# Kernel optimization log

Hardware: AMD Instinct MI355X
Metric: run time of the kernel (lower is better)

Reference implementation:

```python
import jax, jax.numpy as jnp
import numpy as np

B, S, E, H = 2, 2048, 1024, 16
DH = E // H
SCALE = 1.0 / float(np.sqrt(E))  # note: original scales by 1/sqrt(hidden_dim), not head_dim


def _icl_mask(s):
    # triu(diagonal=0) is masked (-inf): only strictly-past positions visible,
    # except (0,0) which is explicitly unmasked so row 0 attends to itself.
    m = jnp.triu(jnp.ones((s, s), dtype=bool), k=0)
    return m.at[0, 0].set(False)


def setup_inputs() -> dict:
    key = jax.random.key(0)
    ks = jax.random.split(key, 7)
    mk = lambda k, shp: jax.random.normal(k, shp, dtype=jnp.float32)
    return {
        "q": mk(ks[0], (B, S, E)),
        "k": mk(ks[1], (B, S, E)),
        "v": mk(ks[2], (B, S, E)),
        "Wq": mk(ks[3], (E, E)) * 0.02,
        "Wk": mk(ks[4], (E, E)) * 0.02,
        "Wv": mk(ks[5], (E, E)) * 0.02,
        "Wo": mk(ks[6], (E, E)) * 0.02,
    }


def reference(q, k, v, Wq, Wk, Wv, Wo):
    b, s, e = q.shape
    h, dh = H, e // H
    # projections (nn.Linear: x @ W.T), split heads -> [b, h, s, dh]
    qh = (q @ Wq.T).reshape(b, s, h, dh).transpose(0, 2, 1, 3)
    kh = (k @ Wk.T).reshape(b, s, h, dh).transpose(0, 2, 1, 3)
    vh = (v @ Wv.T).reshape(b, s, h, dh).transpose(0, 2, 1, 3)
    scores = jnp.einsum("bhsd,bhtd->bhst", qh, kh) * SCALE  # [b,h,s,s]
    scores = jnp.where(_icl_mask(s), -jnp.inf, scores)
    probs = jax.nn.softmax(scores, axis=-1)
    out = jnp.einsum("bhst,bhtd->bhsd", probs, vh)
    out = out.transpose(0, 2, 1, 3).reshape(b, s, e)
    return out @ Wo.T
```

## Files before the change

### kernel.cpp

```cpp
#include <hip/hip_runtime.h>
#include <hip/hip_bf16.h>

typedef unsigned short u16;
typedef unsigned int u32;
typedef __bf16 bf16x8 __attribute__((ext_vector_type(8)));
typedef float float4_ __attribute__((ext_vector_type(4)));

#define B_ 2
#define S_ 2048
#define E_ 1024
#define H_ 16
#define DH_ 64
#define M_ (B_*S_)
#define SCALE_ 0.03125f
#define LOG2E_ 1.4426950408889634f

__device__ __forceinline__ u16 f2bf(float f) {
    unsigned int x = __float_as_uint(f);
    x += 0x7fffu + ((x >> 16) & 1u);
    return (u16)(x >> 16);
}

template <typename T> struct raw8;
template <> struct raw8<float> { float4_ lo, hi; };
template <> struct raw8<u16>   { bf16x8 v; };

__device__ __forceinline__ raw8<float> ldr8(const float* p) {
    raw8<float> r; const float4_* q = (const float4_*)p; r.lo = q[0]; r.hi = q[1]; return r;
}
__device__ __forceinline__ raw8<u16> ldr8(const u16* p) {
    raw8<u16> r; r.v = *(const bf16x8*)p; return r;
}
__device__ __forceinline__ bf16x8 cvt8(const raw8<u16>& r) { return r.v; }
__device__ __forceinline__ bf16x8 cvt8(const raw8<float>& r) {
    union { bf16x8 v; __hip_bfloat162 h[4]; } u;
    u.h[0] = __float22bfloat162_rn(float2{r.lo[0], r.lo[1]});
    u.h[1] = __float22bfloat162_rn(float2{r.lo[2], r.lo[3]});
    u.h[2] = __float22bfloat162_rn(float2{r.hi[0], r.hi[1]});
    u.h[3] = __float22bfloat162_rn(float2{r.hi[2], r.hi[3]});
    return u.v;
}
__device__ __forceinline__ bf16x8 ld8(const u16* p) { return *(const bf16x8*)p; }

__device__ __forceinline__ void async16(u16* lds, const u16* g) {
    __builtin_amdgcn_global_load_lds(
        (const __attribute__((address_space(1))) u32*)g,
        (__attribute__((address_space(3))) u32*)lds, 16, 0, 0);
}

__global__ __launch_bounds__(256)
void convw_kernel(const float* __restrict__ Wq, const float* __restrict__ Wk,
                  const float* __restrict__ Wv, const float* __restrict__ Wo,
                  u16* __restrict__ Wqb, u16* __restrict__ Wkb,
                  u16* __restrict__ Wvb, u16* __restrict__ Wob) {
    const int which = blockIdx.y;
    const float* src = which == 0 ? Wq : which == 1 ? Wk : which == 2 ? Wv : Wo;
    u16* dst        = which == 0 ? Wqb : which == 1 ? Wkb : which == 2 ? Wvb : Wob;
    size_t off = ((size_t)blockIdx.x * 256 + threadIdx.x) * 8;
    *(bf16x8*)&dst[off] = cvt8(ldr8(&src[off]));
}

__global__ __launch_bounds__(256)
void proj_kernel(const float* __restrict__ q, const float* __restrict__ k, const float* __restrict__ v,
                 const u16* __restrict__ Wqb, const u16* __restrict__ Wkb, const u16* __restrict__ Wvb,
                 u16* __restrict__ Qh, u16* __restrict__ Kh, u16* __restrict__ Vt) {
    const int z = blockIdx.z;
    const float* A = (z == 0) ? q : (z == 1) ? k : v;
    const u16* Wb  = (z == 0) ? Wqb : (z == 1) ? Wkb : Wvb;
    u16* C         = (z == 0) ? Qh : (z == 1) ? Kh : Vt;
    const float cscale = (z == 0) ? SCALE_ : 1.0f;
    const int transV = (z == 2);
    const int bm = blockIdx.x * 128, bn = blockIdx.y * 128;

    __shared__ u16 As[128 * 32];
    __shared__ u16 Bs[128 * 32];

    const int tid  = threadIdx.x;
    const int lane = tid & 63;
    const int w    = tid >> 6;
    const int wr   = (w >> 1) * 64, wc = (w & 1) * 64;
    const int m16  = lane & 15, quad = lane >> 4, q4 = quad * 4;
    const int row0 = tid >> 2, kc0 = (tid & 3) * 8, row1 = row0 + 64;
    const int c1   = tid + 256;

    u16* bs_d0 = (u16*)((char*)Bs + (size_t)tid * 16);
    u16* bs_d1 = (u16*)((char*)Bs + (size_t)c1 * 16);
    const u16* wg0 = &Wb[(size_t)(bn + (tid >> 2)) * 1024 + (tid & 3) * 8];
    const u16* wg1 = &Wb[(size_t)(bn + (c1 >> 2)) * 1024 + (c1 & 3) * 8];

    float4_ acc[4][4];
#pragma unroll
    for (int i = 0; i < 4; i++)
#pragma unroll
        for (int j = 0; j < 4; j++) acc[i][j] = (float4_){0.f, 0.f, 0.f, 0.f};

    raw8<float> pa0 = ldr8(&A[(size_t)(bm + row0) * 1024 + kc0]);
    raw8<float> pa1 = ldr8(&A[(size_t)(bm + row1) * 1024 + kc0]);

    for (int k0 = 0; k0 < 1024; k0 += 32) {
        __syncthreads();
        async16(bs_d0, wg0 + k0);
        async16(bs_d1, wg1 + k0);
        *(bf16x8*)&As[row0 * 32 + kc0] = cvt8(pa0);
        *(bf16x8*)&As[row1 * 32 + kc0] = cvt8(pa1);
        __syncthreads();
        if (k0 + 32 < 1024) {
            pa0 = ldr8(&A[(size_t)(bm + row0) * 1024 + k0 + 32 + kc0]);
            pa1 = ldr8(&A[(size_t)(bm + row1) * 1024 + k0 + 32 + kc0]);
        }
        bf16x8 af[4], bfr[4];
#pragma unroll
        for (int rt = 0; rt < 4; rt++)
            af[rt] = *(const bf16x8*)&As[(wr + rt * 16 + m16) * 32 + quad * 8];
#pragma unroll
        for (int ct = 0; ct < 4; ct++)
            bfr[ct] = *(const bf16x8*)&Bs[(wc + ct * 16 + m16) * 32 + quad * 8];
#pragma unroll
        for (int rt = 0; rt < 4; rt++)
#pragma unroll
            for (int ct = 0; ct < 4; ct++)
                acc[rt][ct] = __builtin_amdgcn_mfma_f32_16x16x32_bf16(af[rt], bfr[ct], acc[rt][ct], 0, 0, 0);
    }

#pragma unroll
    for (int rt = 0; rt < 4; rt++)
#pragma unroll
        for (int ct = 0; ct < 4; ct++)
#pragma unroll
            for (int r = 0; r < 4; r++) {
                int row = bm + wr + rt * 16 + q4 + r;
                int col = bn + wc + ct * 16 + m16;
                u16 val = f2bf(acc[rt][ct][r] * cscale);
                if (!transV) {
                    C[(size_t)row * 1024 + col] = val;
                } else {
                    int bb = row >> 11, s = row & 2047;
                    C[((size_t)(bb * 1024 + col)) * 2048 + s] = val;
                }
            }
}

__global__ __launch_bounds__(256)
void out_kernel(const u16* __restrict__ AO, const u16* __restrict__ Wob, float* __restrict__ C) {
    const int bm = blockIdx.x * 128, bn = blockIdx.y * 64;

    __shared__ u16 As[128 * 32];
    __shared__ u16 Bs[64 * 32];

    const int tid  = threadIdx.x;
    const int lane = tid & 63;
    const int w    = tid >> 6;
    const int m16  = lane & 15, quad = lane >> 4, q4 = quad * 4;
    const int c1   = tid + 256;

    u16* as_d0 = (u16*)((char*)As + (size_t)tid * 16);
    u16* as_d1 = (u16*)((char*)As + (size_t)c1 * 16);
    u16* bs_d  = (u16*)((char*)Bs + (size_t)tid * 16);
    const u16* ag0 = &AO[(size_t)(bm + (tid >> 2)) * 1024 + (tid & 3) * 8];
    const u16* ag1 = &AO[(size_t)(bm + (c1 >> 2)) * 1024 + (c1 & 3) * 8];
    const u16* bg  = &Wob[(size_t)(bn + (tid >> 2)) * 1024 + (tid & 3) * 8];

    float4_ acc[2][4];
#pragma unroll
    for (int i = 0; i < 2; i++)
#pragma unroll
        for (int j = 0; j < 4; j++) acc[i][j] = (float4_){0.f, 0.f, 0.f, 0.f};

    for (int k0 = 0; k0 < 1024; k0 += 32) {
        __syncthreads();
        async16(as_d0, ag0 + k0);
        async16(as_d1, ag1 + k0);
        async16(bs_d,  bg  + k0);
        __syncthreads();

        bf16x8 af[2], bfr[4];
#pragma unroll
        for (int rt = 0; rt < 2; rt++)
            af[rt] = *(const bf16x8*)&As[(w * 32 + rt * 16 + m16) * 32 + quad * 8];
#pragma unroll
        for (int ct = 0; ct < 4; ct++)
            bfr[ct] = *(const bf16x8*)&Bs[(ct * 16 + m16) * 32 + quad * 8];
#pragma unroll
        for (int rt = 0; rt < 2; rt++)
#pragma unroll
            for (int ct = 0; ct < 4; ct++)
                acc[rt][ct] = __builtin_amdgcn_mfma_f32_16x16x32_bf16(af[rt], bfr[ct], acc[rt][ct], 0, 0, 0);
    }

#pragma unroll
    for (int rt = 0; rt < 2; rt++)
#pragma unroll
        for (int ct = 0; ct < 4; ct++)
#pragma unroll
            for (int r = 0; r < 4; r++) {
                int row = bm + w * 32 + rt * 16 + q4 + r;
                int col = bn + ct * 16 + m16;
                C[(size_t)row * 1024 + col] = acc[rt][ct][r];
            }
}

__device__ __forceinline__ int sw64(int row, int col) {
    return row * 64 + ((((col >> 3) ^ (row & 7)) << 3) | (col & 7));
}

__global__ __launch_bounds__(256)
void attn_kernel(const u16* __restrict__ Qh, const u16* __restrict__ Kh,
                 const u16* __restrict__ Vt, u16* __restrict__ O) {
    const int h    = blockIdx.x;
    const int pair = blockIdx.y;
    const int tqA  = pair;
    const int tqB  = 31 - pair;
    const int b    = blockIdx.z;
    const int tid  = threadIdx.x;
    const int lane = tid & 63;
    const int w    = tid >> 6;
    const int m16  = lane & 15;
    const int quad = lane >> 4;
    const int q4   = quad * 4;

    __shared__ u16 Ks[2][64 * 64];
    __shared__ u16 Vs[2][64 * 64];
    __shared__ u16 PsA[64 * 64];
    __shared__ u16 PsB[64 * 64];

    const int srow0 = tid >> 3;
    const int skc0  = (tid & 7) * 8;
    const int sblk0 = ((skc0 >> 3) ^ (srow0 & 7)) << 3;
    const int srow1 = srow0 + 32;
    const int sblk1 = ((skc0 >> 3) ^ (srow1 & 7)) << 3;

    const size_t kbase = ((size_t)(b * S_)) * E_ + h * DH_;
    const size_t vbase = ((size_t)(b * 1024 + h * DH_)) * 2048;

    bf16x8 qfA[2], qfB[2];
    {
        const u16* qa = Qh + ((size_t)(b * S_ + tqA * 64 + w * 16 + m16)) * E_ + h * DH_;
        const u16* qb = Qh + ((size_t)(b * S_ + tqB * 64 + w * 16 + m16)) * E_ + h * DH_;
        qfA[0] = ld8(qa + quad * 8);  qfA[1] = ld8(qa + 32 + quad * 8);
        qfB[0] = ld8(qb + quad * 8);  qfB[1] = ld8(qb + 32 + quad * 8);
    }

    float lA[4] = {0.f, 0.f, 0.f, 0.f}, lB[4] = {0.f, 0.f, 0.f, 0.f};
    float4_ oA[4], oB[4];
#pragma unroll
    for (int dt = 0; dt < 4; dt++) { oA[dt] = (float4_){0.f,0.f,0.f,0.f}; oB[dt] = (float4_){0.f,0.f,0.f,0.f}; }

    *(bf16x8*)&Ks[0][srow0 * 64 + sblk0] = ld8(&Kh[kbase + (size_t)srow0 * E_ + skc0]);
    *(bf16x8*)&Ks[0][srow1 * 64 + sblk1] = ld8(&Kh[kbase + (size_t)srow1 * E_ + skc0]);
    *(bf16x8*)&Vs[0][srow0 * 64 + sblk0] = ld8(&Vt[vbase + (size_t)srow0 * 2048 + skc0]);
    *(bf16x8*)&Vs[0][srow1 * 64 + sblk1] = ld8(&Vt[vbase + (size_t)srow1 * 2048 + skc0]);
    __syncthreads();

    for (int t = 0; t <= tqB; t++) {
        const int cur = t & 1;

        bf16x8 kr0, kr1, vr0, vr1;
        const bool havepf = (t < tqB);
        if (havepf) {
            const size_t ko = kbase + (size_t)((t + 1) * 64) * E_;
            kr0 = ld8(&Kh[ko + (size_t)srow0 * E_ + skc0]);
            kr1 = ld8(&Kh[ko + (size_t)srow1 * E_ + skc0]);
            vr0 = ld8(&Vt[vbase + (size_t)srow0 * 2048 + (t + 1) * 64 + skc0]);
            vr1 = ld8(&Vt[vbase + (size_t)srow1 * 2048 + (t + 1) * 64 + skc0]);
        }

        auto process = [&](const bf16x8* qf, float* l_part, float4_* o_acc,
                           u16* Ps, int tqX) {
            const u16* Kc = &Ks[cur][0];
            const u16* Vc = &Vs[cur][0];
            float4_ sc[4];
#pragma unroll
            for (int ct = 0; ct < 4; ct++) sc[ct] = (float4_){0.f,0.f,0.f,0.f};
#pragma unroll
            for (int ks = 0; ks < 2; ks++)
#pragma unroll
                for (int ct = 0; ct < 4; ct++) {
                    bf16x8 kf = *(const bf16x8*)&Kc[sw64(ct * 16 + m16, ks * 32 + quad * 8)];
                    sc[ct] = __builtin_amdgcn_mfma_f32_16x16x32_bf16(qf[ks], kf, sc[ct], 0, 0, 0);
                }

            float p[4][4];
            if (t != tqX) {
#pragma unroll
                for (int ct = 0; ct < 4; ct++)
#pragma unroll
                    for (int r = 0; r < 4; r++) {
                        float pp = exp2f(sc[ct][r] * LOG2E_);
                        p[ct][r] = pp;
                        l_part[r] += pp;
                    }
            } else {
#pragma unroll
                for (int ct = 0; ct < 4; ct++)
#pragma unroll
                    for (int r = 0; r < 4; r++) {
                        int i_loc = w * 16 + q4 + r;
                        int j_loc = ct * 16 + m16;
                        bool allow = (j_loc < i_loc) || (tqX == 0 && i_loc == 0 && j_loc == 0);
                        float pp = allow ? exp2f(sc[ct][r] * LOG2E_) : 0.f;
                        p[ct][r] = pp;
                        l_part[r] += pp;
                    }
            }

#pragma unroll
            for (int ct = 0; ct < 4; ct++)
#pragma unroll
                for (int r = 0; r < 4; r++)
                    Ps[sw64(w * 16 + q4 + r, ct * 16 + m16)] = f2bf(p[ct][r]);

#pragma unroll
            for (int ks = 0; ks < 2; ks++) {
                bf16x8 pf = *(const bf16x8*)&Ps[sw64(w * 16 + m16, ks * 32 + quad * 8)];
#pragma unroll
                for (int dt = 0; dt < 4; dt++) {
                    bf16x8 vf = *(const bf16x8*)&Vc[sw64(dt * 16 + m16, ks * 32 + quad * 8)];
                    o_acc[dt] = __builtin_amdgcn_mfma_f32_16x16x32_bf16(pf, vf, o_acc[dt], 0, 0, 0);
                }
            }
        };

        process(qfB, lB, oB, PsB, tqB);
        if (t <= tqA) process(qfA, lA, oA, PsA, tqA);

        if (havepf) {
            const int nxt = cur ^ 1;
            *(bf16x8*)&Ks[nxt][srow0 * 64 + sblk0] = kr0;
            *(bf16x8*)&Ks[nxt][srow1 * 64 + sblk1] = kr1;
            *(bf16x8*)&Vs[nxt][srow0 * 64 + sblk0] = vr0;
            *(bf16x8*)&Vs[nxt][srow1 * 64 + sblk1] = vr1;
        }
        __syncthreads();
    }

    auto wrout = [&](const float4_* o_acc, const float* l_part, int tqX) {
        const size_t obase = ((size_t)(b * S_ + tqX * 64)) * E_ + h * DH_;
#pragma unroll
        for (int r = 0; r < 4; r++) {
            float l = l_part[r];
#pragma unroll
            for (int msk = 1; msk <= 8; msk <<= 1) l += __shfl_xor(l, msk);
            float inv_l = 1.0f / l;
            int row = w * 16 + q4 + r;
#pragma unroll
            for (int dt = 0; dt < 4; dt++) {
                int col = dt * 16 + m16;
                O[obase + (size_t)row * E_ + col] = f2bf(o_acc[dt][r] * inv_l);
            }
        }
    };
    wrout(oA, lA, tqA);
    wrout(oB, lB, tqB);
}

extern "C" void kernel_launch(void* const* d_in, const int* in_sizes, int n_in,
                              void* d_out, int out_size, void* d_ws, size_t ws_size,
                              hipStream_t stream) {
    const float* q  = (const float*)d_in[0];
    const float* k  = (const float*)d_in[1];
    const float* v  = (const float*)d_in[2];
    const float* Wq = (const float*)d_in[3];
    const float* Wk = (const float*)d_in[4];
    const float* Wv = (const float*)d_in[5];
    const float* Wo = (const float*)d_in[6];

    u16* ws  = (u16*)d_ws;
    u16* Qh  = ws;
    u16* Kh  = ws + (size_t)M_ * E_;
    u16* Vt  = ws + 2 * (size_t)M_ * E_;
    u16* AO  = ws + 3 * (size_t)M_ * E_;
    u16* Wqb = AO;
    u16* Wkb = AO + (size_t)E_ * E_;
    u16* Wvb = AO + 2 * (size_t)E_ * E_;
    u16* Wob = ws + 4 * (size_t)M_ * E_;

    dim3 blk(256);
    convw_kernel<<<dim3(512, 4), blk, 0, stream>>>(Wq, Wk, Wv, Wo, Wqb, Wkb, Wvb, Wob);
    proj_kernel<<<dim3(32, 8, 3), blk, 0, stream>>>(q, k, v, Wqb, Wkb, Wvb, Qh, Kh, Vt);
    attn_kernel<<<dim3(16, 16, 2), blk, 0, stream>>>(Qh, Kh, Vt, AO);
    out_kernel<<<dim3(32, 16), blk, 0, stream>>>(AO, Wob, (float*)d_out);
}
```

Before: 218.2 us.

## Double-buffer LDS tiles in projection and output GEMMs

Both the QKV projection and output projection GEMMs now keep two LDS buffers per operand. The next K-tile is issued into the alternate buffer while MFMAs run on the current one, which removes one of the two barriers per iteration. The goal is to hide global-load latency behind compute. The cost is twice the LDS footprint, which may lower occupancy.

Measured after the change: 247.6 us. 1.13x slower.

```diff
diff --git a/kernel.cpp b/kernel.cpp
--- a/kernel.cpp
+++ b/kernel.cpp
@@ -72,8 +72,8 @@
     const int transV = (z == 2);
     const int bm = blockIdx.x * 128, bn = blockIdx.y * 128;
 
-    __shared__ u16 As[128 * 32];
-    __shared__ u16 Bs[128 * 32];
+    __shared__ u16 As[2][128 * 32];
+    __shared__ u16 Ws[2][128 * 32];
 
     const int tid  = threadIdx.x;
     const int lane = tid & 63;
@@ -83,10 +83,10 @@
     const int row0 = tid >> 2, kc0 = (tid & 3) * 8, row1 = row0 + 64;
     const int c1   = tid + 256;
 
-    u16* bs_d0 = (u16*)((char*)Bs + (size_t)tid * 16);
-    u16* bs_d1 = (u16*)((char*)Bs + (size_t)c1 * 16);
     const u16* wg0 = &Wb[(size_t)(bn + (tid >> 2)) * 1024 + (tid & 3) * 8];
     const u16* wg1 = &Wb[(size_t)(bn + (c1 >> 2)) * 1024 + (c1 & 3) * 8];
+    const float* ag0 = &A[(size_t)(bm + row0) * 1024 + kc0];
+    const float* ag1 = &A[(size_t)(bm + row1) * 1024 + kc0];
 
     float4_ acc[4][4];
 #pragma unroll
@@ -94,32 +94,44 @@
 #pragma unroll
         for (int j = 0; j < 4; j++) acc[i][j] = (float4_){0.f, 0.f, 0.f, 0.f};
 
-    raw8<float> pa0 = ldr8(&A[(size_t)(bm + row0) * 1024 + kc0]);
-    raw8<float> pa1 = ldr8(&A[(size_t)(bm + row1) * 1024 + kc0]);
+    async16((u16*)((char*)&Ws[0][0] + (size_t)tid * 16), wg0);
+    async16((u16*)((char*)&Ws[0][0] + (size_t)c1 * 16),  wg1);
+    raw8<float> pa0 = ldr8(ag0), pa1 = ldr8(ag1);
+    *(bf16x8*)&As[0][row0 * 32 + kc0] = cvt8(pa0);
+    *(bf16x8*)&As[0][row1 * 32 + kc0] = cvt8(pa1);
+    pa0 = ldr8(ag0 + 32); pa1 = ldr8(ag1 + 32);
+    __syncthreads();
 
     for (int k0 = 0; k0 < 1024; k0 += 32) {
-        __syncthreads();
-        async16(bs_d0, wg0 + k0);
-        async16(bs_d1, wg1 + k0);
-        *(bf16x8*)&As[row0 * 32 + kc0] = cvt8(pa0);
-        *(bf16x8*)&As[row1 * 32 + kc0] = cvt8(pa1);
-        __syncthreads();
-        if (k0 + 32 < 1024) {
-            pa0 = ldr8(&A[(size_t)(bm + row0) * 1024 + k0 + 32 + kc0]);
-            pa1 = ldr8(&A[(size_t)(bm + row1) * 1024 + k0 + 32 + kc0]);
+        const int cur = (k0 >> 5) & 1, nxt = cur ^ 1;
+        const int kn = k0 + 32;
+
+        bf16x8 af[4], bfr[4];
+#pragma unroll
+        for (int rt = 0; rt < 4; rt++)
+            af[rt] = *(const bf16x8*)&As[cur][(wr + rt * 16 + m16) * 32 + quad * 8];
+#pragma unroll
+        for (int ct = 0; ct < 4; ct++)
+            bfr[ct] = *(const bf16x8*)&Ws[cur][(wc + ct * 16 + m16) * 32 + quad * 8];
+
+        if (kn < 1024) {
+            async16((u16*)((char*)&Ws[nxt][0] + (size_t)tid * 16), wg0 + kn);
+            async16((u16*)((char*)&Ws[nxt][0] + (size_t)c1 * 16),  wg1 + kn);
+            *(bf16x8*)&As[nxt][row0 * 32 + kc0] = cvt8(pa0);
+            *(bf16x8*)&As[nxt][row1 * 32 + kc0] = cvt8(pa1);
+            if (k0 + 64 < 1024) {
+                pa0 = ldr8(ag0 + k0 + 64);
+                pa1 = ldr8(ag1 + k0 + 64);
+            }
         }
-        bf16x8 af[4], bfr[4];
-#pragma unroll
-        for (int rt = 0; rt < 4; rt++)
-            af[rt] = *(const bf16x8*)&As[(wr + rt * 16 + m16) * 32 + quad * 8];
-#pragma unroll
-        for (int ct = 0; ct < 4; ct++)
-            bfr[ct] = *(const bf16x8*)&Bs[(wc + ct * 16 + m16) * 32 + quad * 8];
+
 #pragma unroll
         for (int rt = 0; rt < 4; rt++)
 #pragma unroll
             for (int ct = 0; ct < 4; ct++)
                 acc[rt][ct] = __builtin_amdgcn_mfma_f32_16x16x32_bf16(af[rt], bfr[ct], acc[rt][ct], 0, 0, 0);
+
+        if (kn < 1024) __syncthreads();
     }
 
 #pragma unroll
@@ -144,8 +156,8 @@
 void out_kernel(const u16* __restrict__ AO, const u16* __restrict__ Wob, float* __restrict__ C) {
     const int bm = blockIdx.x * 128, bn = blockIdx.y * 64;
 
-    __shared__ u16 As[128 * 32];
-    __shared__ u16 Bs[64 * 32];
+    __shared__ u16 As[2][128 * 32];
+    __shared__ u16 Bs[2][64 * 32];
 
     const int tid  = threadIdx.x;
     const int lane = tid & 63;
@@ -153,9 +165,6 @@
     const int m16  = lane & 15, quad = lane >> 4, q4 = quad * 4;
     const int c1   = tid + 256;
 
-    u16* as_d0 = (u16*)((char*)As + (size_t)tid * 16);
-    u16* as_d1 = (u16*)((char*)As + (size_t)c1 * 16);
-    u16* bs_d  = (u16*)((char*)Bs + (size_t)tid * 16);
     const u16* ag0 = &AO[(size_t)(bm + (tid >> 2)) * 1024 + (tid & 3) * 8];
     const u16* ag1 = &AO[(size_t)(bm + (c1 >> 2)) * 1024 + (c1 & 3) * 8];
     const u16* bg  = &Wob[(size_t)(bn + (tid >> 2)) * 1024 + (tid & 3) * 8];
@@ -166,25 +175,36 @@
 #pragma unroll
         for (int j = 0; j < 4; j++) acc[i][j] = (float4_){0.f, 0.f, 0.f, 0.f};
 
+    async16((u16*)((char*)&As[0][0] + (size_t)tid * 16), ag0);
+    async16((u16*)((char*)&As[0][0] + (size_t)c1 * 16),  ag1);
+    async16((u16*)((char*)&Bs[0][0] + (size_t)tid * 16), bg);
+    __syncthreads();
+
     for (int k0 = 0; k0 < 1024; k0 += 32) {
-        __syncthreads();
-        async16(as_d0, ag0 + k0);
-        async16(as_d1, ag1 + k0);
-        async16(bs_d,  bg  + k0);
-        __syncthreads();
+        const int cur = (k0 >> 5) & 1, nxt = cur ^ 1;
+        const int kn = k0 + 32;
 
         bf16x8 af[2], bfr[4];
 #pragma unroll
         for (int rt = 0; rt < 2; rt++)
-            af[rt] = *(const bf16x8*)&As[(w * 32 + rt * 16 + m16) * 32 + quad * 8];
+            af[rt] = *(const bf16x8*)&As[cur][(w * 32 + rt * 16 + m16) * 32 + quad * 8];
 #pragma unroll
         for (int ct = 0; ct < 4; ct++)
-            bfr[ct] = *(const bf16x8*)&Bs[(ct * 16 + m16) * 32 + quad * 8];
+            bfr[ct] = *(const bf16x8*)&Bs[cur][(ct * 16 + m16) * 32 + quad * 8];
+
+        if (kn < 1024) {
+            async16((u16*)((char*)&As[nxt][0] + (size_t)tid * 16), ag0 + kn);
+            async16((u16*)((char*)&As[nxt][0] + (size_t)c1 * 16),  ag1 + kn);
+            async16((u16*)((char*)&Bs[nxt][0] + (size_t)tid * 16), bg  + kn);
+        }
+
 #pragma unroll
         for (int rt = 0; rt < 2; rt++)
 #pragma unroll
             for (int ct = 0; ct < 4; ct++)
                 acc[rt][ct] = __builtin_amdgcn_mfma_f32_16x16x32_bf16(af[rt], bfr[ct], acc[rt][ct], 0, 0, 0);
+
+        if (kn < 1024) __syncthreads();
     }
 
 #pragma unroll
```

## Replace async LDS loads with register-prefetched swizzled LDS stores in GEMMs

Applied to the files above, without the earlier changes.

The projection and output GEMMs no longer use global_load_lds direct-to-LDS copies. Each thread now prefetches the next K-tile into registers while the current tile is computed, then writes it to LDS using an XOR swizzle on the 16-byte chunk index. The MFMA fragment reads apply the same swizzle, which is meant to cut LDS bank conflicts and hide global load latency behind compute. The cost is extra registers and explicit LDS store instructions per iteration.

New measurement: 241.5 us. 1.11x slower.

```diff
diff --git a/kernel.cpp b/kernel.cpp
--- a/kernel.cpp
+++ b/kernel.cpp
@@ -41,12 +41,6 @@
     return u.v;
 }
 __device__ __forceinline__ bf16x8 ld8(const u16* p) { return *(const bf16x8*)p; }
-
-__device__ __forceinline__ void async16(u16* lds, const u16* g) {
-    __builtin_amdgcn_global_load_lds(
-        (const __attribute__((address_space(1))) u32*)g,
-        (__attribute__((address_space(3))) u32*)lds, 16, 0, 0);
-}
 
 __global__ __launch_bounds__(256)
 void convw_kernel(const float* __restrict__ Wq, const float* __restrict__ Wk,
@@ -58,6 +52,10 @@
     u16* dst        = which == 0 ? Wqb : which == 1 ? Wkb : which == 2 ? Wvb : Wob;
     size_t off = ((size_t)blockIdx.x * 256 + threadIdx.x) * 8;
     *(bf16x8*)&dst[off] = cvt8(ldr8(&src[off]));
+}
+
+__device__ __forceinline__ int ldsoff(int row, int j) {
+    return row * 32 + ((j ^ ((row >> 1) & 3)) & 3) * 8;
 }
 
 __global__ __launch_bounds__(256)
@@ -73,20 +71,21 @@
     const int bm = blockIdx.x * 128, bn = blockIdx.y * 128;
 
     __shared__ u16 As[128 * 32];
-    __shared__ u16 Bs[128 * 32];
+    __shared__ u16 Ws[128 * 32];
 
     const int tid  = threadIdx.x;
     const int lane = tid & 63;
     const int w    = tid >> 6;
     const int wr   = (w >> 1) * 64, wc = (w & 1) * 64;
     const int m16  = lane & 15, quad = lane >> 4, q4 = quad * 4;
-    const int row0 = tid >> 2, kc0 = (tid & 3) * 8, row1 = row0 + 64;
-    const int c1   = tid + 256;
-
-    u16* bs_d0 = (u16*)((char*)Bs + (size_t)tid * 16);
-    u16* bs_d1 = (u16*)((char*)Bs + (size_t)c1 * 16);
-    const u16* wg0 = &Wb[(size_t)(bn + (tid >> 2)) * 1024 + (tid & 3) * 8];
-    const u16* wg1 = &Wb[(size_t)(bn + (c1 >> 2)) * 1024 + (c1 & 3) * 8];
+    const int r0   = tid >> 2, j0 = tid & 3, kc0 = j0 * 8;
+    const int st0  = ldsoff(r0, j0);
+    const int sjf  = (m16 >> 1) & 3;
+
+    const float* ag0 = &A[(size_t)(bm + r0) * 1024 + kc0];
+    const float* ag1 = &A[(size_t)(bm + r0 + 64) * 1024 + kc0];
+    const u16*   wg0 = &Wb[(size_t)(bn + r0) * 1024 + kc0];
+    const u16*   wg1 = &Wb[(size_t)(bn + r0 + 64) * 1024 + kc0];
 
     float4_ acc[4][4];
 #pragma unroll
@@ -94,27 +93,29 @@
 #pragma unroll
         for (int j = 0; j < 4; j++) acc[i][j] = (float4_){0.f, 0.f, 0.f, 0.f};
 
-    raw8<float> pa0 = ldr8(&A[(size_t)(bm + row0) * 1024 + kc0]);
-    raw8<float> pa1 = ldr8(&A[(size_t)(bm + row1) * 1024 + kc0]);
+    raw8<float> pa0 = ldr8(ag0), pa1 = ldr8(ag1);
+    bf16x8      pw0 = ld8(wg0),  pw1 = ld8(wg1);
 
     for (int k0 = 0; k0 < 1024; k0 += 32) {
         __syncthreads();
-        async16(bs_d0, wg0 + k0);
-        async16(bs_d1, wg1 + k0);
-        *(bf16x8*)&As[row0 * 32 + kc0] = cvt8(pa0);
-        *(bf16x8*)&As[row1 * 32 + kc0] = cvt8(pa1);
+        *(bf16x8*)&As[st0]           = cvt8(pa0);
+        *(bf16x8*)&As[st0 + 64 * 32] = cvt8(pa1);
+        *(bf16x8*)&Ws[st0]           = pw0;
+        *(bf16x8*)&Ws[st0 + 64 * 32] = pw1;
         __syncthreads();
         if (k0 + 32 < 1024) {
-            pa0 = ldr8(&A[(size_t)(bm + row0) * 1024 + k0 + 32 + kc0]);
-            pa1 = ldr8(&A[(size_t)(bm + row1) * 1024 + k0 + 32 + kc0]);
+            pa0 = ldr8(ag0 + k0 + 32);
+            pa1 = ldr8(ag1 + k0 + 32);
+            pw0 = ld8(wg0 + k0 + 32);
+            pw1 = ld8(wg1 + k0 + 32);
         }
         bf16x8 af[4], bfr[4];
 #pragma unroll
         for (int rt = 0; rt < 4; rt++)
-            af[rt] = *(const bf16x8*)&As[(wr + rt * 16 + m16) * 32 + quad * 8];
+            af[rt] = *(const bf16x8*)&As[(wr + rt * 16 + m16) * 32 + ((quad ^ sjf) & 3) * 8];
 #pragma unroll
         for (int ct = 0; ct < 4; ct++)
-            bfr[ct] = *(const bf16x8*)&Bs[(wc + ct * 16 + m16) * 32 + quad * 8];
+            bfr[ct] = *(const bf16x8*)&Ws[(wc + ct * 16 + m16) * 32 + ((quad ^ sjf) & 3) * 8];
 #pragma unroll
         for (int rt = 0; rt < 4; rt++)
 #pragma unroll
@@ -151,14 +152,13 @@
     const int lane = tid & 63;
     const int w    = tid >> 6;
     const int m16  = lane & 15, quad = lane >> 4, q4 = quad * 4;
-    const int c1   = tid + 256;
-
-    u16* as_d0 = (u16*)((char*)As + (size_t)tid * 16);
-    u16* as_d1 = (u16*)((char*)As + (size_t)c1 * 16);
-    u16* bs_d  = (u16*)((char*)Bs + (size_t)tid * 16);
-    const u16* ag0 = &AO[(size_t)(bm + (tid >> 2)) * 1024 + (tid & 3) * 8];
-    const u16* ag1 = &AO[(size_t)(bm + (c1 >> 2)) * 1024 + (c1 & 3) * 8];
-    const u16* bg  = &Wob[(size_t)(bn + (tid >> 2)) * 1024 + (tid & 3) * 8];
+    const int r0   = tid >> 2, j0 = tid & 3, kc0 = j0 * 8;
+    const int st0  = ldsoff(r0, j0);
+    const int sjf  = (m16 >> 1) & 3;
+
+    const u16* ag0 = &AO[(size_t)(bm + r0) * 1024 + kc0];
+    const u16* ag1 = &AO[(size_t)(bm + r0 + 64) * 1024 + kc0];
+    const u16* bg  = &Wob[(size_t)(bn + r0) * 1024 + kc0];
 
     float4_ acc[2][4];
 #pragma unroll
@@ -166,20 +166,26 @@
 #pragma unroll
         for (int j = 0; j < 4; j++) acc[i][j] = (float4_){0.f, 0.f, 0.f, 0.f};
 
+    bf16x8 pa0 = ld8(ag0), pa1 = ld8(ag1), pb = ld8(bg);
+
     for (int k0 = 0; k0 < 1024; k0 += 32) {
         __syncthreads();
-        async16(as_d0, ag0 + k0);
-        async16(as_d1, ag1 + k0);
-        async16(bs_d,  bg  + k0);
-        __syncthreads();
-
+        *(bf16x8*)&As[st0]           = pa0;
+        *(bf16x8*)&As[st0 + 64 * 32] = pa1;
+        if (r0 < 64) *(bf16x8*)&Bs[st0] = pb;
+        __syncthreads();
+        if (k0 + 32 < 1024) {
+            pa0 = ld8(ag0 + k0 + 32);
+            pa1 = ld8(ag1 + k0 + 32);
+            pb  = ld8(bg  + k0 + 32);
+        }
         bf16x8 af[2], bfr[4];
 #pragma unroll
         for (int rt = 0; rt < 2; rt++)
-            af[rt] = *(const bf16x8*)&As[(w * 32 + rt * 16 + m16) * 32 + quad * 8];
+            af[rt] = *(const bf16x8*)&As[(w * 32 + rt * 16 + m16) * 32 + ((quad ^ sjf) & 3) * 8];
 #pragma unroll
         for (int ct = 0; ct < 4; ct++)
-            bfr[ct] = *(const bf16x8*)&Bs[(ct * 16 + m16) * 32 + quad * 8];
+            bfr[ct] = *(const bf16x8*)&Bs[(ct * 16 + m16) * 32 + ((quad ^ sjf) & 3) * 8];
 #pragma unroll
         for (int rt = 0; rt < 2; rt++)
 #pragma unroll
```
